# Kernel tuning notes

Measured on AMD Instinct MI355X. Metric: run time of the kernel, lower is better.

Reference implementation:

```python
import jax, jax.numpy as jnp
import numpy as np

B, C, H, W = 4, 8, 384, 384
NUM_LAYERS = 5
CG_ITERS = 10


def conv2d(x, w, b):
    # x: [B,Cin,H,W], w: [Cout,Cin,3,3]
    y = jax.lax.conv_general_dilated(x, w, (1, 1), 'SAME',
                                     dimension_numbers=('NCHW', 'OIHW', 'NCHW'))
    return y + b[None, :, None, None]


def dw(x, w_in, b_in, ws_mid, bs_mid, w_out, b_out):
    # Sequence: conv, conv, relu, conv, conv, relu, conv, conv, relu, conv, conv, relu, conv
    h = conv2d(x, w_in, b_in)
    for i in range(7):
        h = conv2d(h, ws_mid[i], bs_mid[i])
        if i % 2 == 0:  # ReLU after convs 2,4,6,8
            h = jax.nn.relu(h)
    h = conv2d(h, w_out, b_out)
    return x + h  # residual


def conjugate_grad(rhs, csm_c, mask, lam):
    # rhs: [B,H,W] complex; csm_c: [B,C,H,W] complex; mask: [B,H,W] real
    def AtA(p):
        coil = csm_c * p[:, None]                      # [B,C,H,W]
        k = jnp.fft.fft2(coil) * mask[:, None]         # masked k-space
        return jnp.sum(jnp.conj(csm_c) * jnp.fft.ifft2(k), axis=1)

    def body(carry, _):
        x, r, p, rTr = carry
        Ap = AtA(p) + lam * p
        pAp = jnp.sum(jnp.conj(p) * Ap, axis=(-2, -1)).real
        alpha = rTr / pAp
        x = x + alpha[:, None, None] * p
        r = r - alpha[:, None, None] * Ap
        rTrNew = jnp.sum(jnp.conj(r) * r, axis=(-2, -1)).real
        beta = rTrNew / rTr
        p = r + beta[:, None, None] * p
        return (x, r, p, rTrNew), None

    x0 = jnp.zeros_like(rhs)
    rTr0 = jnp.sum(jnp.conj(rhs) * rhs, axis=(-2, -1)).real
    (x, _, _, _), _ = jax.lax.scan(body, (x0, rhs, rhs, rTr0), None, length=CG_ITERS)
    return x


def reference(under_img, csm, mask, lam, w_in, b_in, ws_mid, bs_mid, w_out, b_out):
    csm_c = jax.lax.complex(csm[..., 0], csm[..., 1])  # [B,C,H,W] complex
    lam_s = lam[0]
    x = under_img
    for _ in range(NUM_LAYERS):
        x = dw(x, w_in, b_in, ws_mid, bs_mid, w_out, b_out)
        x = under_img + lam_s * x
        rhs = jax.lax.complex(x[:, 0], x[:, 1])        # view_as_complex(permute(0,2,3,1))
        xc = conjugate_grad(rhs, csm_c, mask, lam_s)
        x = jnp.stack([xc.real, xc.imag], axis=1)      # view_as_real -> [B,2,H,W]
    return x


def setup_inputs() -> dict:
    key = jax.random.key(0)
    ks = jax.random.split(key, 8)
    under_img = jax.random.normal(ks[0], (B, 2, H, W), jnp.float32)
    csm = jax.random.normal(ks[1], (B, C, H, W, 2), jnp.float32) / np.sqrt(C)
    mask = (jax.random.uniform(ks[2], (B, H, W)) > 0.5).astype(jnp.float32)
    lam = jnp.array([0.05], jnp.float32)
    w_in = jax.random.normal(ks[3], (64, 2, 3, 3), jnp.float32) * 0.02
    b_in = jnp.zeros((64,), jnp.float32)
    ws_mid = jax.random.normal(ks[4], (7, 64, 64, 3, 3), jnp.float32) * 0.02
    bs_mid = jnp.zeros((7, 64), jnp.float32)
    w_out = jax.random.normal(ks[5], (2, 64, 3, 3), jnp.float32) * 0.02
    b_out = jnp.zeros((2,), jnp.float32)
    return {"under_img": under_img, "csm": csm, "mask": mask, "lam": lam,
            "w_in": w_in, "b_in": b_in, "ws_mid": ws_mid, "bs_mid": bs_mid,
            "w_out": w_out, "b_out": b_out}
```

## Files before the change

### kernel.cpp

```cpp
#include <hip/hip_runtime.h>
#include <hip/hip_bf16.h>
#include <math.h>

#define HH 384
#define WW 384
#define HW (HH*WW)
#define BB 4
#define CC 8
#define NLAYERS 5
#define CGITERS 10
#define PI_F 3.14159265358979323846f

typedef __attribute__((ext_vector_type(8))) short short8;
typedef __attribute__((ext_vector_type(4))) float floatx4;

struct cf { float x, y; };
__device__ __forceinline__ cf cadd(cf a, cf b){ cf r; r.x=a.x+b.x; r.y=a.y+b.y; return r; }
__device__ __forceinline__ cf csub(cf a, cf b){ cf r; r.x=a.x-b.x; r.y=a.y-b.y; return r; }
__device__ __forceinline__ cf cmul(cf a, cf b){ cf r; r.x=a.x*b.x - a.y*b.y; r.y=a.x*b.y + a.y*b.x; return r; }
__device__ __forceinline__ cf shflxor(cf v, int m){ cf r; r.x = __shfl_xor(v.x, m); r.y = __shfl_xor(v.y, m); return r; }
__device__ __forceinline__ int brev7(int l){ return (int)(__brev((unsigned)l) >> 25); }
__device__ __forceinline__ int padi(int i){ return i + (i >> 3); }

__device__ __forceinline__ void radix3(cf a0, cf a1, cf a2, float s3, cf y[3]) {
  float tx = a1.x + a2.x, ty_ = a1.y + a2.y;
  float ux = a1.x - a2.x, uy = a1.y - a2.y;
  y[0].x = a0.x + tx;              y[0].y = a0.y + ty_;
  y[1].x = a0.x - 0.5f*tx - s3*uy; y[1].y = a0.y - 0.5f*ty_ + s3*ux;
  y[2].x = a0.x - 0.5f*tx + s3*uy; y[2].y = a0.y - 0.5f*ty_ - s3*ux;
}

template<int SIGN>
__device__ __forceinline__ void fft384_wave(int l, const cf v[6], cf uA[3], cf uB[3]) {
  const float s3 = SIGN * 0.8660254037844386f;
  radix3(v[0], v[2], v[4], s3, uA);
  radix3(v[1], v[3], v[5], s3, uB);
  const float base = SIGN * (2.0f * PI_F / 384.0f);
  float sA, cA; __sincosf(base * (float)l, &sA, &cA);
  cf wA1; wA1.x = cA; wA1.y = sA; cf wA2 = cmul(wA1, wA1);
  float sB, cB; __sincosf(base * (float)(l + 64), &sB, &cB);
  cf wB1; wB1.x = cB; wB1.y = sB; cf wB2 = cmul(wB1, wB1);
  uA[1] = cmul(uA[1], wA1); uA[2] = cmul(uA[2], wA2);
  uB[1] = cmul(uB[1], wB1); uB[2] = cmul(uB[2], wB2);
  {
    float s, c; __sincosf(SIGN * (PI_F/64.0f) * (float)l, &s, &c);
    cf w; w.x = c; w.y = s;
    #pragma unroll
    for (int k1 = 0; k1 < 3; ++k1) {
      cf a = uA[k1], b = uB[k1];
      uA[k1] = cadd(a, b);
      uB[k1] = cmul(csub(a, b), w);
    }
  }
  #pragma unroll
  for (int h = 32; h >= 1; h >>= 1) {
    const int j = l & (h - 1);
    float s, c; __sincosf(SIGN * PI_F * (float)j / (float)h, &s, &c);
    cf w; w.x = c; w.y = s;
    const bool up = (l & h) != 0;
    #pragma unroll
    for (int k1 = 0; k1 < 3; ++k1) {
      cf pa = shflxor(uA[k1], h);
      cf pb = shflxor(uB[k1], h);
      cf na = up ? cmul(csub(pa, uA[k1]), w) : cadd(uA[k1], pa);
      cf nb = up ? cmul(csub(pb, uB[k1]), w) : cadd(uB[k1], pb);
      uA[k1] = na; uB[k1] = nb;
    }
  }
}


__global__ void repack_mid_k(const float* __restrict__ ws_mid, __hip_bfloat16* __restrict__ wrep) {
  const int idx = blockIdx.x * 256 + threadIdx.x;
  if (idx >= 7*9*64*64) return;
  const int ci = idx & 63, co = (idx >> 6) & 63, tap = (idx >> 12) % 9, i = idx / (9*4096);
  wrep[idx] = __float2bfloat16(ws_mid[(((size_t)i*64 + co)*64 + ci)*9 + tap]);
}

__global__ void __launch_bounds__(256) conv_in_k(const float* __restrict__ xin,
                                                 const float* __restrict__ w,
                                                 const float* __restrict__ bias,
                                                 __hip_bfloat16* __restrict__ out) {
  __shared__ float tile[2][340];
  const int tx = threadIdx.x & 31, ty = threadIdx.x >> 5;
  const int x0 = blockIdx.x * 32, y0 = blockIdx.y * 8, b = blockIdx.z;
  for (int e = threadIdx.x; e < 680; e += 256) {
    int ci = e / 340, rr = e % 340;
    int iy = y0 - 1 + rr / 34, ix = x0 - 1 + rr % 34;
    float v = 0.f;
    if (iy >= 0 && iy < HH && ix >= 0 && ix < WW)
      v = xin[(b*2 + ci)*HW + iy*WW + ix];
    tile[ci][rr] = v;
  }
  __syncthreads();
  float acc[64];
  #pragma unroll
  for (int co = 0; co < 64; ++co) acc[co] = bias[co];
  #pragma unroll
  for (int ci = 0; ci < 2; ++ci) {
    float v0 = tile[ci][ty*34+tx],     v1 = tile[ci][ty*34+tx+1],     v2 = tile[ci][ty*34+tx+2];
    float v3 = tile[ci][(ty+1)*34+tx], v4 = tile[ci][(ty+1)*34+tx+1], v5 = tile[ci][(ty+1)*34+tx+2];
    float v6 = tile[ci][(ty+2)*34+tx], v7 = tile[ci][(ty+2)*34+tx+1], v8 = tile[ci][(ty+2)*34+tx+2];
    #pragma unroll
    for (int co = 0; co < 64; ++co) {
      const float* wp = w + co*18 + ci*9;
      float a = acc[co];
      a = fmaf(v0, wp[0], a); a = fmaf(v1, wp[1], a); a = fmaf(v2, wp[2], a);
      a = fmaf(v3, wp[3], a); a = fmaf(v4, wp[4], a); a = fmaf(v5, wp[5], a);
      a = fmaf(v6, wp[6], a); a = fmaf(v7, wp[7], a); a = fmaf(v8, wp[8], a);
      acc[co] = a;
    }
  }
  const size_t obase = ((size_t)(b*HH + y0 + ty)*WW + (x0 + tx))*64;
  #pragma unroll
  for (int s = 0; s < 8; ++s) {
    uint4 u;
    __hip_bfloat16* hp = (__hip_bfloat16*)&u;
    #pragma unroll
    for (int j = 0; j < 8; ++j) hp[j] = __float2bfloat16(acc[s*8 + j]);
    *(uint4*)(out + obase + s*8) = u;
  }
}

__global__ void __launch_bounds__(256) conv_mid_mfma_k(
    const __hip_bfloat16* __restrict__ in,
    const __hip_bfloat16* __restrict__ wrep,
    const float* __restrict__ bias,
    __hip_bfloat16* __restrict__ out, int relu) {
  __shared__ __hip_bfloat16 atile[6*34*72];
  const int tid = threadIdx.x;
  const int l = tid & 63, wv = tid >> 6;
  const int x0 = blockIdx.x * 32, y0 = blockIdx.y * 4, b = blockIdx.z;

  for (int e = tid; e < 204*8; e += 256) {
    int p = e >> 3, s = e & 7;
    int iy = y0 - 1 + p / 34, ix = x0 - 1 + p % 34;
    uint4 v = make_uint4(0u, 0u, 0u, 0u);
    if (iy >= 0 && iy < HH && ix >= 0 && ix < WW)
      v = *(const uint4*)(in + ((size_t)(b*HH + iy)*WW + ix)*64 + s*8);
    *(uint4*)(&atile[p*72 + s*8]) = v;
  }

  floatx4 acc[2][4];
  #pragma unroll
  for (int mt = 0; mt < 2; ++mt)
    #pragma unroll
    for (int nt = 0; nt < 4; ++nt)
      acc[mt][nt] = (floatx4){0.f, 0.f, 0.f, 0.f};

  const int kseg = l >> 4;
  const int lr = l & 15;

  __syncthreads();

  #pragma unroll 1
  for (int tap = 0; tap < 9; ++tap) {
    const int dy = tap / 3, dx = tap - dy*3;
    const __hip_bfloat16* wt = wrep + tap*4096 + lr*64 + kseg*8;
    short8 bf[4][2];
    #pragma unroll
    for (int nt = 0; nt < 4; ++nt) {
      bf[nt][0] = *(const short8*)(wt + nt*1024);
      bf[nt][1] = *(const short8*)(wt + nt*1024 + 32);
    }
    short8 af[2][2];
    #pragma unroll
    for (int mt = 0; mt < 2; ++mt) {
      const int py = wv + dy;
      const int px = mt*16 + lr + dx;
      const __hip_bfloat16* ap = &atile[(py*34 + px)*72 + kseg*8];
      af[mt][0] = *(const short8*)(ap);
      af[mt][1] = *(const short8*)(ap + 32);
    }
    #pragma unroll
    for (int mt = 0; mt < 2; ++mt)
      #pragma unroll
      for (int nt = 0; nt < 4; ++nt) {
        acc[mt][nt] = __builtin_amdgcn_mfma_f32_16x16x32_bf16(af[mt][0], bf[nt][0], acc[mt][nt], 0, 0, 0);
        acc[mt][nt] = __builtin_amdgcn_mfma_f32_16x16x32_bf16(af[mt][1], bf[nt][1], acc[mt][nt], 0, 0, 0);
      }
  }

  __syncthreads();
  __hip_bfloat16* otile = atile;
  #pragma unroll
  for (int mt = 0; mt < 2; ++mt) {
    #pragma unroll
    for (int nt = 0; nt < 4; ++nt) {
      const int ch = nt*16 + lr;
      const float bv = bias[ch];
      #pragma unroll
      for (int rr = 0; rr < 4; ++rr) {
        const int px = mt*16 + kseg*4 + rr;
        float v = acc[mt][nt][rr] + bv;
        if (relu) v = fmaxf(v, 0.f);
        otile[(wv*32 + px)*72 + ch] = __float2bfloat16(v);
      }
    }
  }
  __syncthreads();
  #pragma unroll
  for (int iter = 0; iter < 4; ++iter) {
    const int e = iter*256 + tid;
    const int p = e >> 3, s = e & 7;
    const int row = p >> 5, px = p & 31;
    uint4 v = *(const uint4*)(&otile[p*72 + s*8]);
    *(uint4*)(out + ((size_t)(b*HH + y0 + row)*WW + (x0 + px))*64 + s*8) = v;
  }
}

__global__ void __launch_bounds__(256) conv_out_k(const __hip_bfloat16* __restrict__ in,
                                                  const float* __restrict__ w,
                                                  const float* __restrict__ bias,
                                                  const float* __restrict__ xcur,
                                                  const float* __restrict__ under,
                                                  const float* __restrict__ lam,
                                                  cf* __restrict__ r, cf* __restrict__ p,
                                                  cf* __restrict__ xc, float* __restrict__ scL) {
  __shared__ __hip_bfloat16 atile[340*72];
  __shared__ float wl[2*64*9];
  __shared__ float wsum[4];
  const int tid = threadIdx.x;
  const int tx = tid & 31, ty = tid >> 5;
  const int x0 = blockIdx.x * 32, y0 = blockIdx.y * 8, b = blockIdx.z;

  for (int e = tid; e < 340*8; e += 256) {
    int pp = e >> 3, s = e & 7;
    int iy = y0 - 1 + pp / 34, ix = x0 - 1 + pp % 34;
    uint4 v = make_uint4(0u, 0u, 0u, 0u);
    if (iy >= 0 && iy < HH && ix >= 0 && ix < WW)
      v = *(const uint4*)(in + ((size_t)(b*HH + iy)*WW + ix)*64 + s*8);
    *(uint4*)(&atile[pp*72 + s*8]) = v;
  }
  for (int e = tid; e < 2*64*9; e += 256) wl[e] = w[e];
  __syncthreads();

  float a0 = bias[0], a1 = bias[1];
  #pragma unroll 1
  for (int tap = 0; tap < 9; ++tap) {
    const int dy = tap / 3, dx = tap - dy*3;
    const __hip_bfloat16* ap = &atile[((ty + dy)*34 + tx + dx)*72];
    #pragma unroll
    for (int s = 0; s < 8; ++s) {
      short8 v8 = *(const short8*)(ap + s*8);
      const __hip_bfloat16* hv = (const __hip_bfloat16*)&v8;
      #pragma unroll
      for (int j = 0; j < 8; ++j) {
        const float f = __bfloat162float(hv[j]);
        a0 = fmaf(f, wl[(s*8 + j)*9 + tap], a0);
        a1 = fmaf(f, wl[(64 + s*8 + j)*9 + tap], a1);
      }
    }
  }
  const float lamv = lam[0];
  const int y = y0 + ty, x = x0 + tx;
  const int idx2 = y*WW + x;
  float xv0 = xcur[b*2*HW + idx2],  xv1 = xcur[b*2*HW + HW + idx2];
  float u0  = under[b*2*HW + idx2], u1  = under[b*2*HW + HW + idx2];
  float r0 = u0 + lamv * (xv0 + a0);
  float r1 = u1 + lamv * (xv1 + a1);
  const int cidx = b*HW + idx2;
  cf vv; vv.x = r0; vv.y = r1;
  r[cidx] = vv; p[cidx] = vv;
  cf zz; zz.x = 0.f; zz.y = 0.f; xc[cidx] = zz;
  float partial = r0*r0 + r1*r1;
  for (int off = 32; off; off >>= 1) partial += __shfl_down(partial, off);
  const int l = tid & 63, wvid = tid >> 6;
  if (l == 0) wsum[wvid] = partial;
  __syncthreads();
  if (tid == 0) atomicAdd(&scL[b], wsum[0]+wsum[1]+wsum[2]+wsum[3]);
}


__global__ void __launch_bounds__(256) pass_a_k(const cf* __restrict__ rold, cf* __restrict__ rnew,
                                                const cf* __restrict__ pold, cf* __restrict__ pnew,
                                                cf* __restrict__ xc, const cf* __restrict__ Ap,
                                                const cf* __restrict__ csm, cf* __restrict__ t,
                                                float* __restrict__ scL, int it) {
  __shared__ cf rowbuf[4][434];
  const int l = threadIdx.x & 63, wv = threadIdx.x >> 6;
  const int y = blockIdx.x * 4 + wv;
  const int c = blockIdx.y, b = blockIdx.z;
  const int rowoff = b*HW + y*WW;
  cf pv[6];
  if (it == 0) {
    #pragma unroll
    for (int m = 0; m < 6; ++m) pv[m] = pold[rowoff + l + 64*m];
  } else {
    const float rtrp  = scL[(it-1)*4 + b];
    const float pApp  = scL[40 + (it-1)*4 + b];
    const float ApApp = scL[80 + (it-1)*4 + b];
    const float alpha = rtrp / pApp;
    const float rtrn  = alpha*alpha*ApApp - rtrp;
    const float beta  = rtrn / rtrp;
    if (blockIdx.x == 0 && c == 0 && threadIdx.x == 0) scL[it*4 + b] = rtrn;
    #pragma unroll
    for (int m = 0; m < 6; ++m) {
      const int idx = rowoff + l + 64*m;
      cf rv = rold[idx];
      cf av = Ap[idx];
      rv.x -= alpha*av.x; rv.y -= alpha*av.y;
      cf po = pold[idx];
      pv[m].x = rv.x + beta*po.x; pv[m].y = rv.y + beta*po.y;
      if (c == 0) {
        rnew[idx] = rv;
        pnew[idx] = pv[m];
        cf xv = xc[idx]; xv.x += alpha*po.x; xv.y += alpha*po.y; xc[idx] = xv;
      }
    }
  }
  const cf* crow = csm + (b*CC + c)*HW + y*WW;
  cf v[6];
  #pragma unroll
  for (int m = 0; m < 6; ++m) v[m] = cmul(crow[l + 64*m], pv[m]);
  cf uA[3], uB[3];
  fft384_wave<-1>(l, v, uA, uB);
  const int R3 = 3 * brev7(l);
  cf* rb = rowbuf[wv];
  #pragma unroll
  for (int k1 = 0; k1 < 3; ++k1) { rb[padi(k1 + R3)] = uA[k1]; rb[padi(k1 + R3 + 3)] = uB[k1]; }
  cf* trow = t + (b*CC + c)*HW + y*WW;
  #pragma unroll
  for (int m = 0; m < 6; ++m) trow[l + 64*m] = rb[padi(l + 64*m)];
}

__global__ void __launch_bounds__(256) pass_b_k(cf* __restrict__ t, const float* __restrict__ mask) {
  __shared__ cf tile[431*9];
  const int b = blockIdx.z, c = blockIdx.y, x0 = blockIdx.x * 8;
  cf* base = t + (b*CC + c)*HW;
  for (int e = threadIdx.x; e < 3072; e += 256) {
    int y = e >> 3, xx = e & 7;
    tile[padi(y)*9 + xx] = base[y*WW + x0 + xx];
  }
  __syncthreads();
  const int l = threadIdx.x & 63, wv = threadIdx.x >> 6;
  const int R3 = 3 * brev7(l);
  for (int rep = 0; rep < 2; ++rep) {
    const int xx = wv*2 + rep, x = x0 + xx;
    cf v[6];
    #pragma unroll
    for (int m = 0; m < 6; ++m) v[m] = tile[padi(l + 64*m)*9 + xx];
    cf uA[3], uB[3];
    fft384_wave<-1>(l, v, uA, uB);
    const float* mrow = mask + b*HW + x;
    #pragma unroll
    for (int k1 = 0; k1 < 3; ++k1) {
      float mA = mrow[(k1 + R3)*WW], mB = mrow[(k1 + R3 + 3)*WW];
      uA[k1].x *= mA; uA[k1].y *= mA; uB[k1].x *= mB; uB[k1].y *= mB;
    }
    __syncthreads();
    #pragma unroll
    for (int k1 = 0; k1 < 3; ++k1) { tile[padi(k1 + R3)*9 + xx] = uA[k1]; tile[padi(k1 + R3 + 3)*9 + xx] = uB[k1]; }
    __syncthreads();
    #pragma unroll
    for (int m = 0; m < 6; ++m) v[m] = tile[padi(l + 64*m)*9 + xx];
    fft384_wave<1>(l, v, uA, uB);
    const float s = 1.0f / 384.0f;
    #pragma unroll
    for (int k1 = 0; k1 < 3; ++k1) {
      uA[k1].x *= s; uA[k1].y *= s; uB[k1].x *= s; uB[k1].y *= s;
      tile[padi(k1 + R3)*9 + xx] = uA[k1]; tile[padi(k1 + R3 + 3)*9 + xx] = uB[k1];
    }
    __syncthreads();
  }
  for (int e = threadIdx.x; e < 3072; e += 256) {
    int y = e >> 3, xx = e & 7;
    base[y*WW + x0 + xx] = tile[padi(y)*9 + xx];
  }
}

__global__ void __launch_bounds__(256) pass_c_k(const cf* __restrict__ t, const cf* __restrict__ csm,
                                                const cf* __restrict__ p, cf* __restrict__ Ap,
                                                const float* __restrict__ lam,
                                                float* __restrict__ scL, int it) {
  __shared__ cf rowbuf[4][434];
  __shared__ cf redbuf[3][384];
  const int l = threadIdx.x & 63, wv = threadIdx.x >> 6;
  const int y = blockIdx.x, b = blockIdx.y;
  const int R3 = 3 * brev7(l);
  cf* rb = rowbuf[wv];
  cf acc[6] = {};
  #pragma unroll 1
  for (int ci = 0; ci < 2; ++ci) {
    const int c = wv*2 + ci;
    const cf* trow = t + (b*CC + c)*HW + y*WW;
    cf v[6];
    #pragma unroll
    for (int m = 0; m < 6; ++m) v[m] = trow[l + 64*m];
    cf uA[3], uB[3];
    fft384_wave<1>(l, v, uA, uB);
    #pragma unroll
    for (int k1 = 0; k1 < 3; ++k1) { rb[padi(k1 + R3)] = uA[k1]; rb[padi(k1 + R3 + 3)] = uB[k1]; }
    const cf* crow = csm + (b*CC + c)*HW + y*WW;
    #pragma unroll
    for (int m = 0; m < 6; ++m) {
      cf cs = crow[l + 64*m];
      cf wz = rb[padi(l + 64*m)];
      acc[m].x += cs.x*wz.x + cs.y*wz.y;
      acc[m].y += cs.x*wz.y - cs.y*wz.x;
    }
  }
  if (wv > 0) {
    #pragma unroll
    for (int m = 0; m < 6; ++m) redbuf[wv - 1][l + 64*m] = acc[m];
  }
  __syncthreads();
  if (wv == 0) {
    #pragma unroll
    for (int m = 0; m < 6; ++m) {
      #pragma unroll
      for (int j = 0; j < 3; ++j) {
        cf o = redbuf[j][l + 64*m];
        acc[m].x += o.x; acc[m].y += o.y;
      }
    }
    const float lamv = lam[0];
    const float sc384 = 1.0f / 384.0f;
    const cf* prow = p + b*HW + y*WW;
    cf* aprow = Ap + b*HW + y*WW;
    float partial = 0.f, partial2 = 0.f;
    #pragma unroll
    for (int m = 0; m < 6; ++m) {
      cf pv = prow[l + 64*m];
      cf ap; ap.x = acc[m].x*sc384 + lamv*pv.x; ap.y = acc[m].y*sc384 + lamv*pv.y;
      aprow[l + 64*m] = ap;
      partial  += pv.x*ap.x + pv.y*ap.y;
      partial2 += ap.x*ap.x + ap.y*ap.y;
    }
    #pragma unroll
    for (int off = 32; off; off >>= 1) {
      partial  += __shfl_down(partial, off);
      partial2 += __shfl_down(partial2, off);
    }
    if (l == 0) {
      atomicAdd(&scL[40 + it*4 + b], partial);
      atomicAdd(&scL[80 + it*4 + b], partial2);
    }
  }
}

__global__ void __launch_bounds__(256) final_x_k(const cf* __restrict__ xc, const cf* __restrict__ p9,
                                                 const float* __restrict__ scL, float* __restrict__ out) {
  const int idx = blockIdx.x * 256 + threadIdx.x;
  const int b = idx / HW;
  const int rem = idx - b*HW;
  const float alpha = scL[(CGITERS-1)*4 + b] / scL[40 + (CGITERS-1)*4 + b];
  cf xv = xc[idx], pv = p9[idx];
  xv.x += alpha*pv.x; xv.y += alpha*pv.y;
  out[b*2*HW + rem] = xv.x;
  out[b*2*HW + HW + rem] = xv.y;
}

__global__ void zero_sc_k(float* sc) {
  for (int i = threadIdx.x; i < NLAYERS*128; i += 256) sc[i] = 0.f;
}

extern "C" void kernel_launch(void* const* d_in, const int* in_sizes, int n_in,
                              void* d_out, int out_size, void* d_ws, size_t ws_size,
                              hipStream_t stream) {
  (void)in_sizes; (void)n_in; (void)out_size; (void)ws_size;
  const float* under  = (const float*)d_in[0];
  const cf*    csm    = (const cf*)d_in[1];
  const float* mask   = (const float*)d_in[2];
  const float* lam    = (const float*)d_in[3];
  const float* w_in   = (const float*)d_in[4];
  const float* b_in   = (const float*)d_in[5];
  const float* ws_mid = (const float*)d_in[6];
  const float* bs_mid = (const float*)d_in[7];
  const float* w_out  = (const float*)d_in[8];
  const float* b_out  = (const float*)d_in[9];
  float* xcur = (float*)d_out;

  char* bws = (char*)d_ws;
  size_t off = 0;
  auto carve = [&](size_t bytes) { char* pp = bws + off; off += (bytes + 255) & ~(size_t)255; return (void*)pp; };
  __hip_bfloat16* actA = (__hip_bfloat16*)carve((size_t)BB*64*HW*2);
  __hip_bfloat16* actB = (__hip_bfloat16*)carve((size_t)BB*64*HW*2);
  cf* t     = (cf*)carve((size_t)BB*CC*HW*8);
  cf* rbuf0 = (cf*)carve((size_t)BB*HW*8);
  cf* rbuf1 = (cf*)carve((size_t)BB*HW*8);
  cf* pbuf0 = (cf*)carve((size_t)BB*HW*8);
  cf* pbuf1 = (cf*)carve((size_t)BB*HW*8);
  cf* xc    = (cf*)carve((size_t)BB*HW*8);
  cf* Ap    = (cf*)carve((size_t)BB*HW*8);
  float* sc = (float*)carve(4096);
  __hip_bfloat16* wrep = (__hip_bfloat16*)carve((size_t)7*9*64*64*2);

  hipMemcpyAsync(xcur, under, (size_t)BB*2*HW*sizeof(float), hipMemcpyDeviceToDevice, stream);

  zero_sc_k<<<1, 256, 0, stream>>>(sc);
  repack_mid_k<<<(7*9*64*64 + 255)/256, 256, 0, stream>>>(ws_mid, wrep);

  dim3 cgrid(WW/32, HH/8, BB);
  dim3 mgrid(WW/32, HH/4, BB);
  dim3 agrid(HH/4, CC, BB);
  dim3 bgrid(WW/8, CC, BB);
  dim3 c2grid(HH, BB);
  const int egrid = BB*HW/256;

  __hip_bfloat16* bufs[2] = { actA, actB };
  cf* rb[2] = { rbuf0, rbuf1 };
  cf* pb[2] = { pbuf0, pbuf1 };

  for (int layer = 0; layer < NLAYERS; ++layer) {
    float* scL = sc + layer*128;
    conv_in_k<<<cgrid, 256, 0, stream>>>(xcur, w_in, b_in, bufs[0]);
    for (int i = 0; i < 7; ++i) {
      conv_mid_mfma_k<<<mgrid, 256, 0, stream>>>(bufs[i & 1], wrep + (size_t)i*9*4096,
                                                 bs_mid + i*64, bufs[(i + 1) & 1], (i % 2 == 0) ? 1 : 0);
    }
    conv_out_k<<<cgrid, 256, 0, stream>>>(bufs[1], w_out, b_out, xcur, under, lam,
                                          rbuf0, pbuf0, xc, scL);
    for (int it = 0; it < CGITERS; ++it) {
      cf* rold = rb[(it + 1) & 1];
      cf* rnew = rb[it & 1];
      cf* pold = pb[(it + 1) & 1];
      cf* pnew = pb[it & 1];
      if (it == 0) { rold = rbuf0; pold = pbuf0; rnew = rbuf0; pnew = pbuf0; }
      pass_a_k<<<agrid, 256, 0, stream>>>(rold, rnew, pold, pnew, xc, Ap, csm, t, scL, it);
      pass_b_k<<<bgrid, 256, 0, stream>>>(t, mask);
      pass_c_k<<<c2grid, 256, 0, stream>>>(t, csm, pnew, Ap, lam, scL, it);
    }
    final_x_k<<<egrid, 256, 0, stream>>>(xc, pb[(CGITERS - 1) & 1], scL, xcur);
  }
}
```

Baseline: 11.05 ms.

## Enlarge mid-conv tile to 8 rows, prefetch weights, and use twiddle recurrences in FFT

The MFMA 64-channel conv now computes 8 output rows per block instead of 4, with each wave handling two rows. This shrinks the relative halo reload and reuses each weight fragment across twice as many MFMAs. Next-tap weights are prefetched into registers while the current tap's MFMAs run. The radix-384 FFT replaces most __sincosf calls with twiddles built by squaring and multiplying from one base twiddle, and flips the butterfly subtraction to match. The costs are more accumulator and weight registers, which may lower occupancy, and slightly different FFT rounding from the recurrence.

```diff
diff --git a/kernel.cpp b/kernel.cpp
--- a/kernel.cpp
+++ b/kernel.cpp
@@ -18,6 +18,7 @@
 __device__ __forceinline__ cf cadd(cf a, cf b){ cf r; r.x=a.x+b.x; r.y=a.y+b.y; return r; }
 __device__ __forceinline__ cf csub(cf a, cf b){ cf r; r.x=a.x-b.x; r.y=a.y-b.y; return r; }
 __device__ __forceinline__ cf cmul(cf a, cf b){ cf r; r.x=a.x*b.x - a.y*b.y; r.y=a.x*b.y + a.y*b.x; return r; }
+__device__ __forceinline__ cf csqr(cf a){ cf r; r.x = a.x*a.x - a.y*a.y; r.y = 2.f*a.x*a.y; return r; }
 __device__ __forceinline__ cf shflxor(cf v, int m){ cf r; r.x = __shfl_xor(v.x, m); r.y = __shfl_xor(v.y, m); return r; }
 __device__ __forceinline__ int brev7(int l){ return (int)(__brev((unsigned)l) >> 25); }
 __device__ __forceinline__ int padi(int i){ return i + (i >> 3); }
@@ -35,35 +36,32 @@
   const float s3 = SIGN * 0.8660254037844386f;
   radix3(v[0], v[2], v[4], s3, uA);
   radix3(v[1], v[3], v[5], s3, uB);
-  const float base = SIGN * (2.0f * PI_F / 384.0f);
-  float sA, cA; __sincosf(base * (float)l, &sA, &cA);
-  cf wA1; wA1.x = cA; wA1.y = sA; cf wA2 = cmul(wA1, wA1);
-  float sB, cB; __sincosf(base * (float)(l + 64), &sB, &cB);
-  cf wB1; wB1.x = cB; wB1.y = sB; cf wB2 = cmul(wB1, wB1);
+  float sA, cA;
+  __sincosf(SIGN * (2.0f * PI_F / 384.0f) * (float)l, &sA, &cA);
+  cf wA1; wA1.x = cA; wA1.y = sA;
+  cf wA2 = csqr(wA1);
+  cf w6; w6.x = 0.5f; w6.y = s3;
+  cf wB1 = cmul(wA1, w6);
+  cf wB2 = csqr(wB1);
   uA[1] = cmul(uA[1], wA1); uA[2] = cmul(uA[2], wA2);
   uB[1] = cmul(uB[1], wB1); uB[2] = cmul(uB[2], wB2);
-  {
-    float s, c; __sincosf(SIGN * (PI_F/64.0f) * (float)l, &s, &c);
-    cf w; w.x = c; w.y = s;
-    #pragma unroll
-    for (int k1 = 0; k1 < 3; ++k1) {
-      cf a = uA[k1], b = uB[k1];
-      uA[k1] = cadd(a, b);
-      uB[k1] = cmul(csub(a, b), w);
-    }
+  cf u = cmul(wA2, wA1);
+  #pragma unroll
+  for (int k1 = 0; k1 < 3; ++k1) {
+    cf a = uA[k1], b = uB[k1];
+    uA[k1] = cadd(a, b);
+    uB[k1] = cmul(csub(a, b), u);
   }
   #pragma unroll
   for (int h = 32; h >= 1; h >>= 1) {
-    const int j = l & (h - 1);
-    float s, c; __sincosf(SIGN * PI_F * (float)j / (float)h, &s, &c);
-    cf w; w.x = c; w.y = s;
+    u = csqr(u);
     const bool up = (l & h) != 0;
     #pragma unroll
     for (int k1 = 0; k1 < 3; ++k1) {
       cf pa = shflxor(uA[k1], h);
       cf pb = shflxor(uB[k1], h);
-      cf na = up ? cmul(csub(pa, uA[k1]), w) : cadd(uA[k1], pa);
-      cf nb = up ? cmul(csub(pb, uB[k1]), w) : cadd(uB[k1], pb);
+      cf na = up ? cmul(csub(uA[k1], pa), u) : cadd(uA[k1], pa);
+      cf nb = up ? cmul(csub(uB[k1], pb), u) : cadd(uB[k1], pb);
       uA[k1] = na; uB[k1] = nb;
     }
   }
@@ -127,12 +125,12 @@
     const __hip_bfloat16* __restrict__ wrep,
     const float* __restrict__ bias,
     __hip_bfloat16* __restrict__ out, int relu) {
-  __shared__ __hip_bfloat16 atile[6*34*72];
+  __shared__ __hip_bfloat16 atile[10*34*72];
   const int tid = threadIdx.x;
   const int l = tid & 63, wv = tid >> 6;
-  const int x0 = blockIdx.x * 32, y0 = blockIdx.y * 4, b = blockIdx.z;
-
-  for (int e = tid; e < 204*8; e += 256) {
+  const int x0 = blockIdx.x * 32, y0 = blockIdx.y * 8, b = blockIdx.z;
+
+  for (int e = tid; e < 340*8; e += 256) {
     int p = e >> 3, s = e & 7;
     int iy = y0 - 1 + p / 34, ix = x0 - 1 + p % 34;
     uint4 v = make_uint4(0u, 0u, 0u, 0u);
@@ -141,9 +139,9 @@
     *(uint4*)(&atile[p*72 + s*8]) = v;
   }
 
-  floatx4 acc[2][4];
-  #pragma unroll
-  for (int mt = 0; mt < 2; ++mt)
+  floatx4 acc[4][4];
+  #pragma unroll
+  for (int mt = 0; mt < 4; ++mt)
     #pragma unroll
     for (int nt = 0; nt < 4; ++nt)
       acc[mt][nt] = (floatx4){0.f, 0.f, 0.f, 0.f};
@@ -151,58 +149,72 @@
   const int kseg = l >> 4;
   const int lr = l & 15;
 
+  const __hip_bfloat16* wlane = wrep + lr*64 + kseg*8;
+  short8 bf[4][2];
+  #pragma unroll
+  for (int nt = 0; nt < 4; ++nt) {
+    bf[nt][0] = *(const short8*)(wlane + nt*1024);
+    bf[nt][1] = *(const short8*)(wlane + nt*1024 + 32);
+  }
+
   __syncthreads();
 
   #pragma unroll 1
   for (int tap = 0; tap < 9; ++tap) {
+    short8 bfn[4][2];
+    if (tap < 8) {
+      const __hip_bfloat16* wn = wlane + (tap + 1)*4096;
+      #pragma unroll
+      for (int nt = 0; nt < 4; ++nt) {
+        bfn[nt][0] = *(const short8*)(wn + nt*1024);
+        bfn[nt][1] = *(const short8*)(wn + nt*1024 + 32);
+      }
+    }
     const int dy = tap / 3, dx = tap - dy*3;
-    const __hip_bfloat16* wt = wrep + tap*4096 + lr*64 + kseg*8;
-    short8 bf[4][2];
-    #pragma unroll
-    for (int nt = 0; nt < 4; ++nt) {
-      bf[nt][0] = *(const short8*)(wt + nt*1024);
-      bf[nt][1] = *(const short8*)(wt + nt*1024 + 32);
-    }
-    short8 af[2][2];
-    #pragma unroll
-    for (int mt = 0; mt < 2; ++mt) {
-      const int py = wv + dy;
-      const int px = mt*16 + lr + dx;
-      const __hip_bfloat16* ap = &atile[(py*34 + px)*72 + kseg*8];
+    short8 af[4][2];
+    #pragma unroll
+    for (int mt = 0; mt < 4; ++mt) {
+      const int ry = 2*wv + (mt >> 1) + dy;
+      const int px = (mt & 1)*16 + lr + dx;
+      const __hip_bfloat16* ap = &atile[(ry*34 + px)*72 + kseg*8];
       af[mt][0] = *(const short8*)(ap);
       af[mt][1] = *(const short8*)(ap + 32);
     }
     #pragma unroll
-    for (int mt = 0; mt < 2; ++mt)
+    for (int mt = 0; mt < 4; ++mt)
       #pragma unroll
       for (int nt = 0; nt < 4; ++nt) {
         acc[mt][nt] = __builtin_amdgcn_mfma_f32_16x16x32_bf16(af[mt][0], bf[nt][0], acc[mt][nt], 0, 0, 0);
         acc[mt][nt] = __builtin_amdgcn_mfma_f32_16x16x32_bf16(af[mt][1], bf[nt][1], acc[mt][nt], 0, 0, 0);
       }
+    if (tap < 8) {
+      #pragma unroll
+      for (int nt = 0; nt < 4; ++nt) { bf[nt][0] = bfn[nt][0]; bf[nt][1] = bfn[nt][1]; }
+    }
   }
 
   __syncthreads();
   __hip_bfloat16* otile = atile;
   #pragma unroll
-  for (int mt = 0; mt < 2; ++mt) {
+  for (int mt = 0; mt < 4; ++mt) {
+    const int row = 2*wv + (mt >> 1);
     #pragma unroll
     for (int nt = 0; nt < 4; ++nt) {
       const int ch = nt*16 + lr;
       const float bv = bias[ch];
       #pragma unroll
       for (int rr = 0; rr < 4; ++rr) {
-        const int px = mt*16 + kseg*4 + rr;
+        const int px = (mt & 1)*16 + kseg*4 + rr;
         float v = acc[mt][nt][rr] + bv;
         if (relu) v = fmaxf(v, 0.f);
-        otile[(wv*32 + px)*72 + ch] = __float2bfloat16(v);
+        otile[(row*32 + px)*72 + ch] = __float2bfloat16(v);
       }
     }
   }
   __syncthreads();
   #pragma unroll
-  for (int iter = 0; iter < 4; ++iter) {
-    const int e = iter*256 + tid;
-    const int p = e >> 3, s = e & 7;
+  for (int iter = 0; iter < 8; ++iter) {
+    const int p = iter*32 + (tid >> 3), s = tid & 7;
     const int row = p >> 5, px = p & 31;
     uint4 v = *(const uint4*)(&otile[p*72 + s*8]);
     *(uint4*)(out + ((size_t)(b*HH + y0 + row)*WW + (x0 + px))*64 + s*8) = v;
@@ -492,7 +504,6 @@
   repack_mid_k<<<(7*9*64*64 + 255)/256, 256, 0, stream>>>(ws_mid, wrep);
 
   dim3 cgrid(WW/32, HH/8, BB);
-  dim3 mgrid(WW/32, HH/4, BB);
   dim3 agrid(HH/4, CC, BB);
   dim3 bgrid(WW/8, CC, BB);
   dim3 c2grid(HH, BB);
@@ -506,7 +517,7 @@
     float* scL = sc + layer*128;
     conv_in_k<<<cgrid, 256, 0, stream>>>(xcur, w_in, b_in, bufs[0]);
     for (int i = 0; i < 7; ++i) {
-      conv_mid_mfma_k<<<mgrid, 256, 0, stream>>>(bufs[i & 1], wrep + (size_t)i*9*4096,
+      conv_mid_mfma_k<<<cgrid, 256, 0, stream>>>(bufs[i & 1], wrep + (size_t)i*9*4096,
                                                  bs_mid + i*64, bufs[(i + 1) & 1], (i % 2 == 0) ? 1 : 0);
     }
     conv_out_k<<<cgrid, 256, 0, stream>>>(bufs[1], w_out, b_out, xcur, under, lam,
```

New measurement: 9.536 ms. -13.7%, faster.
